# Optimization experiments

Measured on AMD Instinct MI355X. Metric: run time of the kernel, lower is better.

Reference implementation:

```python
import jax, jax.numpy as jnp
import numpy as np

B, N, C = 2, 2048, 768
H = 12
D = C // H
SCALE = D ** -0.5
EPS = 1e-5
HID = 4 * C


def layer_norm(x, g, b):
    mu = jnp.mean(x, axis=-1, keepdims=True)
    var = jnp.var(x, axis=-1, keepdims=True)
    return (x - mu) * jax.lax.rsqrt(var + EPS) * g + b


def setup_inputs():
    key = jax.random.key(0)
    ks = jax.random.split(key, 12)
    s = C ** -0.5
    x = jax.random.normal(ks[0], (B, N, C), dtype=jnp.float32)
    mask = (jax.random.uniform(ks[1], (B, N, N)) < 0.1).astype(jnp.float32)
    return {
        "x": x,
        "mask": mask,
        "g1": jnp.ones((C,), jnp.float32),
        "b1": jnp.zeros((C,), jnp.float32),
        "Wq": jax.random.normal(ks[2], (C, C), jnp.float32) * s,
        "Wkv": jax.random.normal(ks[3], (2 * C, C), jnp.float32) * s,
        "Wp": jax.random.normal(ks[4], (C, C), jnp.float32) * s,
        "bp": jnp.zeros((C,), jnp.float32),
        "g2": jnp.ones((C,), jnp.float32),
        "b2": jnp.zeros((C,), jnp.float32),
        "W1": jax.random.normal(ks[5], (HID, C), jnp.float32) * s,
        "bf1": jnp.zeros((HID,), jnp.float32),
        "W2": jax.random.normal(ks[6], (C, HID), jnp.float32) * (HID ** -0.5),
        "bf2": jnpmp if False else jnp.zeros((C,), jnp.float32),
    }


def block_fwd(x, mask, g1, b1, Wq, Wkv, Wp, bp, g2, b2, W1, bf1, W2, bf2):
    # --- attention branch (pre-norm) ---
    xn = layer_norm(x, g1, b1)
    q = (xn @ Wq.T).reshape(B, N, H, D).transpose(0, 2, 1, 3)      # bhnd
    kv = (xn @ Wkv.T).reshape(B, N, 2, H, D).transpose(2, 0, 3, 1, 4)
    k, v = kv[0], kv[1]                                             # bhnd
    attn = jnp.einsum('bhnd,bhmd->bhnm', q, k) * SCALE
    attn = attn + (mask * -100000.0)[:, None]                       # additive mask
    attn = jax.nn.softmax(attn, axis=-1)
    o = jnp.einsum('bhnm,bhmd->bhnd', attn, v)
    o = o.transpose(0, 2, 1, 3).reshape(B, N, C)
    o = o @ Wp.T + bp
    x = x + o
    # --- MLP branch (pre-norm) ---
    xn2 = layer_norm(x, g2, b2)
    h = jax.nn.gelu(xn2 @ W1.T + bf1, approximate=False)
    x = x + (h @ W2.T + bf2)
    return x


def reference(x, mask, g1, b1, Wq, Wkv, Wp, bp, g2, b2, W1, bf1, W2, bf2):
    return block_fwd(x, mask, g1, b1, Wq, Wkv, Wp, bp, g2, b2, W1, bf1, W2, bf2)
```

## Files before the change

### kernel.cpp

```cpp
#include <hip/hip_runtime.h>
#include <hip/hip_bf16.h>
#include <cstdint>
#include <cstddef>

#define BB 2
#define NN 2048
#define CC 768
#define HH 12
#define DD 64
#define HID 3072
#define TT (BB*NN)

typedef __attribute__((ext_vector_type(8))) short bf16x8;
typedef __attribute__((ext_vector_type(4))) short bf16x4;
typedef __attribute__((ext_vector_type(4))) float f32x4;

__device__ __forceinline__ unsigned short f2bf(float f) {
    unsigned int u = __float_as_uint(f);
    u += 0x7fffu + ((u >> 16) & 1u);
    return (unsigned short)(u >> 16);
}
__device__ __forceinline__ float bf2f(unsigned short u) {
    return __uint_as_float(((unsigned int)u) << 16);
}
#if __has_builtin(__builtin_amdgcn_exp2f)
#define EXP2F(x) __builtin_amdgcn_exp2f(x)
#else
#define EXP2F(x) exp2f(x)
#endif

__device__ __forceinline__ void gload16(const void* g, void* l) {
    __builtin_amdgcn_global_load_lds((__attribute__((address_space(1))) unsigned int*)g,
                                     (__attribute__((address_space(3))) unsigned int*)l,
                                     16, 0, 0);
}

#define WAITV(N) asm volatile("s_waitcnt vmcnt(" #N ")" ::: "memory")
#define WAITLGKM asm volatile("s_waitcnt lgkmcnt(0)" ::: "memory")

struct CvtArgs {
    const float* in[5];
    unsigned short* out[5];
    int n4[5];
};
typedef __attribute__((ext_vector_type(4))) float float4v;
typedef __attribute__((ext_vector_type(4))) unsigned short ushort4v;
__global__ __launch_bounds__(256) void cvt5_kernel(CvtArgs a) {
    int base = blockIdx.x * 256 + threadIdx.x;
    int stride = gridDim.x * 256;
#pragma unroll
    for (int s = 0; s < 5; ++s) {
        const float4v* ip = (const float4v*)a.in[s];
        ushort4v* op = (ushort4v*)a.out[s];
        for (int i = base; i < a.n4[s]; i += stride) {
            float4v v = ip[i];
            ushort4v o;
            o[0] = f2bf(v[0]); o[1] = f2bf(v[1]); o[2] = f2bf(v[2]); o[3] = f2bf(v[3]);
            op[i] = o;
        }
    }
}

__global__ __launch_bounds__(256) void maskbits_kernel(const float* __restrict__ mask,
                                                       unsigned short* __restrict__ mb, int n) {
    int i = blockIdx.x * 256 + threadIdx.x;
    if (i >= n) return;
    const float4v* mp = (const float4v*)(mask + (size_t)i * 16);
    unsigned int bits = 0;
#pragma unroll
    for (int q = 0; q < 4; ++q) {
        float4v v = mp[q];
#pragma unroll
        for (int j = 0; j < 4; ++j) bits |= (v[j] > 0.5f) ? (1u << (q * 4 + j)) : 0u;
    }
    mb[i] = (unsigned short)bits;
}

__global__ __launch_bounds__(256) void ln_kernel(const float* __restrict__ x,
                                                 const float* __restrict__ g,
                                                 const float* __restrict__ b,
                                                 unsigned short* __restrict__ out) {
    int t = blockIdx.x;
    int tid = threadIdx.x;
    const float* xr = x + (size_t)t * CC;
    float v0 = xr[tid], v1 = xr[tid + 256], v2 = xr[tid + 512];
    float s = v0 + v1 + v2;
    float s2 = v0 * v0 + v1 * v1 + v2 * v2;
#pragma unroll
    for (int off = 1; off < 64; off <<= 1) {
        s  += __shfl_xor(s, off);
        s2 += __shfl_xor(s2, off);
    }
    __shared__ float red[8];
    int wv = tid >> 6, lane = tid & 63;
    if (lane == 0) { red[wv] = s; red[wv + 4] = s2; }
    __syncthreads();
    s  = red[0] + red[1] + red[2] + red[3];
    s2 = red[4] + red[5] + red[6] + red[7];
    float mu   = s * (1.0f / CC);
    float var  = s2 * (1.0f / CC) - mu * mu;
    float rstd = rsqrtf(var + 1e-5f);
    unsigned short* orow = out + (size_t)t * CC;
    orow[tid]       = f2bf((v0 - mu) * rstd * g[tid]       + b[tid]);
    orow[tid + 256] = f2bf((v1 - mu) * rstd * g[tid + 256] + b[tid + 256]);
    orow[tid + 512] = f2bf((v2 - mu) * rstd * g[tid + 512] + b[tid + 512]);
}

template <int EPI, int BM>
__global__ __launch_bounds__(256) void gemm_bt(const unsigned short* __restrict__ A,
                                               const unsigned short* __restrict__ Bw,
                                               const float* __restrict__ bias,
                                               const float* __restrict__ res,
                                               void* __restrict__ out,
                                               int M, int N, int K) {
    constexpr int MI = BM / 32;
    constexpr int NCA = (BM * 4) / 256;
    __shared__ alignas(16) unsigned short As[2][BM * 32];
    __shared__ alignas(16) unsigned short Bs[2][128 * 32];
    int tid = threadIdx.x;
    int lane = tid & 63, wv = tid >> 6;
    int l16 = lane & 15, lg = lane >> 4;
    int bm = blockIdx.x, bn = blockIdx.y;
    int wm = (wv & 1) * (BM / 2), wn = (wv >> 1) * 64;

    const unsigned short* Ab = A + (size_t)bm * BM * K;
    const unsigned short* Bb = Bw + (size_t)bn * 128 * K;

    const unsigned short* aSrc[NCA]; int aDst[NCA];
#pragma unroll
    for (int i = 0; i < NCA; ++i) {
        int c = tid + i * 256;
        int row = c >> 2, p = c & 3;
        int lc = p ^ ((row >> 1) & 3);
        aSrc[i] = Ab + (size_t)row * K + lc * 8;
        aDst[i] = c * 8;
    }
    const unsigned short* bSrc[2]; int bDst[2];
#pragma unroll
    for (int i = 0; i < 2; ++i) {
        int c = tid + i * 256;
        int row = c >> 2, p = c & 3;
        int lc = p ^ ((row >> 1) & 3);
        bSrc[i] = Bb + (size_t)row * K + lc * 8;
        bDst[i] = c * 8;
    }
    int aoff = (wm + l16) * 32 + ((lg ^ (((wm + l16) >> 1) & 3)) * 8);
    int boff = (wn + l16) * 32 + ((lg ^ (((wn + l16) >> 1) & 3)) * 8);

    f32x4 acc[MI][4];
#pragma unroll
    for (int i = 0; i < MI; ++i)
#pragma unroll
        for (int j = 0; j < 4; ++j) acc[i][j] = f32x4{0.f, 0.f, 0.f, 0.f};

    auto STAGE = [&](int s, int k0) {
#pragma unroll
        for (int i = 0; i < NCA; ++i) gload16(aSrc[i] + k0, &As[s][aDst[i]]);
#pragma unroll
        for (int i = 0; i < 2; ++i)   gload16(bSrc[i] + k0, &Bs[s][bDst[i]]);
    };

    STAGE(0, 0);
    int nt = K / 32;
    for (int t = 0; t < nt; ++t) {
        int cur = t & 1;
        if (t + 1 < nt) {
            STAGE(cur ^ 1, (t + 1) * 32);
            if constexpr (NCA + 2 == 4) { WAITV(4); } else { WAITV(3); }
        } else {
            WAITV(0);
        }
        __builtin_amdgcn_s_barrier();
        bf16x8 af[MI], bfr[4];
#pragma unroll
        for (int mi = 0; mi < MI; ++mi) af[mi]  = *(const bf16x8*)&As[cur][aoff + mi * 512];
#pragma unroll
        for (int ni = 0; ni < 4; ++ni)  bfr[ni] = *(const bf16x8*)&Bs[cur][boff + ni * 512];
#pragma unroll
        for (int mi = 0; mi < MI; ++mi)
#pragma unroll
            for (int ni = 0; ni < 4; ++ni)
                acc[mi][ni] = __builtin_amdgcn_mfma_f32_16x16x32_bf16(bfr[ni], af[mi], acc[mi][ni], 0, 0, 0);
        WAITLGKM;
        __builtin_amdgcn_s_barrier();
    }

#pragma unroll
    for (int mi = 0; mi < MI; ++mi) {
        int row = bm * BM + wm + mi * 16 + l16;
#pragma unroll
        for (int ni = 0; ni < 4; ++ni) {
            int col = bn * 128 + wn + ni * 16 + lg * 4;
            size_t idx = (size_t)row * N + col;
            f32x4 v = acc[mi][ni];
            if (EPI == 0) {
                bf16x4 ov;
#pragma unroll
                for (int r = 0; r < 4; ++r) ov[r] = (short)f2bf(v[r]);
                *(bf16x4*)((unsigned short*)out + idx) = ov;
            } else if (EPI == 1 || EPI == 3) {
                f32x4 bv = *(const f32x4*)&bias[col];
                f32x4 rv = *(const f32x4*)&res[idx];
                f32x4 ov;
#pragma unroll
                for (int r = 0; r < 4; ++r) ov[r] = v[r] + bv[r] + rv[r];
                *(f32x4*)((float*)out + idx) = ov;
            } else {
                f32x4 bv = *(const f32x4*)&bias[col];
                bf16x4 ov;
#pragma unroll
                for (int r = 0; r < 4; ++r) {
                    float t2 = v[r] + bv[r];
                    t2 = 0.5f * t2 * (1.0f + erff(t2 * 0.70710678118f));
                    ov[r] = (short)f2bf(t2);
                }
                *(bf16x4*)((unsigned short*)out + idx) = ov;
            }
        }
    }
}

#define KVB 64
#define ANT (NN/KVB)
#define VP 68
__global__ __launch_bounds__(256, 4) void attn_kernel(const unsigned short* __restrict__ qkv,
                                                      const unsigned short* __restrict__ maskb,
                                                      unsigned short* __restrict__ o) {
    __shared__ alignas(16) unsigned short Ks[2][64 * 64];
    __shared__ alignas(16) unsigned short Vt[2][64 * VP];
    int tid = threadIdx.x;
    int lane = tid & 63, wv = tid >> 6;
    int l16 = lane & 15, lg = lane >> 4;
    int qb = blockIdx.x;
    int bh = blockIdx.y;
    int b = bh / HH, h = bh % HH;
    int qrow = qb * 64 + wv * 16 + l16;

    const unsigned short* qp = qkv + ((size_t)(b * NN + qrow)) * 2304 + h * DD;
    bf16x8 q0r = *(const bf16x8*)(qp + 8 * lg);
    bf16x8 q1r = *(const bf16x8*)(qp + 32 + 8 * lg);
    const float QSC = 0.125f * 1.4426950408889634f;
    bf16x8 q0, q1;
#pragma unroll
    for (int j = 0; j < 8; ++j) {
        q0[j] = (short)f2bf(bf2f((unsigned short)q0r[j]) * QSC);
        q1[j] = (short)f2bf(bf2f((unsigned short)q1r[j]) * QSC);
    }

    const unsigned short* mrow  = maskb + ((size_t)(b * NN + qrow)) * 128;
    const unsigned short* kbase = qkv + (size_t)b * NN * 2304 + 768 + h * DD;
    const unsigned short* vbase = qkv + (size_t)b * NN * 2304 + 1536 + h * DD;

    const unsigned short* kSrc[2]; int kDst[2];
#pragma unroll
    for (int i = 0; i < 2; ++i) {
        int c = tid + i * 256;
        int row = c >> 3, p = c & 7;
        int lc = p ^ (row & 7);
        kSrc[i] = kbase + (size_t)row * 2304 + lc * 8;
        kDst[i] = c * 8;
    }
    int kp = tid & 31, dg = tid >> 5;
    const unsigned short* vSrc = vbase + (size_t)(2 * kp) * 2304 + dg * 8;

    int sw = l16 & 7;
    int kb0 = l16 * 64 + ((lg ^ sw) * 8);
    int kb1 = l16 * 64 + (((lg + 4) ^ sw) * 8);
    int vbo = l16 * VP + lg * 4;

    bf16x8 va, vb;
    unsigned long long mb_cur, mb_nxt;

    f32x4 oa[4];
#pragma unroll
    for (int i = 0; i < 4; ++i) oa[i] = f32x4{0.f, 0.f, 0.f, 0.f};
    float mrun = -INFINITY, lrun = 0.f;

    auto LOAD = [&](int t, int s) {
#pragma unroll
        for (int i = 0; i < 2; ++i) gload16(kSrc[i] + (size_t)t * KVB * 2304, &Ks[s][kDst[i]]);
        const unsigned short* vp = vSrc + (size_t)t * KVB * 2304;
        va = *(const bf16x8*)(vp);
        vb = *(const bf16x8*)(vp + 2304);
        mb_nxt = *(const unsigned long long*)(mrow + t * 4);
    };
    auto WRITEV = [&](int s) {
        unsigned int* VtU = (unsigned int*)Vt[s];
#pragma unroll
        for (int j = 0; j < 8; ++j)
            VtU[(dg * 8 + j) * (VP / 2) + kp] =
                (unsigned int)(unsigned short)va[j] | ((unsigned int)(unsigned short)vb[j] << 16);
    };

    LOAD(0, 0);
    WRITEV(0);
    mb_cur = mb_nxt;
    __syncthreads();
    int cur = 0;

    for (int kt = 0; kt < ANT; ++kt) {
        bool pre = (kt + 1 < ANT);
        if (pre) LOAD(kt + 1, cur ^ 1);
        const unsigned short* Ksc = Ks[cur];
        const unsigned short* Vtc = Vt[cur];

        float sv[16];
#pragma unroll
        for (int ks = 0; ks < 4; ++ks) {
            bf16x8 k0 = *(const bf16x8*)&Ksc[kb0 + ks * 1024];
            bf16x8 k1 = *(const bf16x8*)&Ksc[kb1 + ks * 1024];
            f32x4 sa = f32x4{0.f, 0.f, 0.f, 0.f};
            sa = __builtin_amdgcn_mfma_f32_16x16x32_bf16(k0, q0, sa, 0, 0, 0);
            sa = __builtin_amdgcn_mfma_f32_16x16x32_bf16(k1, q1, sa, 0, 0, 0);
            unsigned int m16 = (unsigned int)(mb_cur >> (ks * 16 + lg * 4));
#pragma unroll
            for (int r = 0; r < 4; ++r) {
                float mbit = (float)((m16 >> r) & 1u);
                sv[ks * 4 + r] = fmaf(mbit, -144269.5f, sa[r]);
            }
        }
        float tmax = sv[0];
#pragma unroll
        for (int i = 1; i < 16; ++i) tmax = fmaxf(tmax, sv[i]);
        tmax = fmaxf(tmax, __shfl_xor(tmax, 16));
        tmax = fmaxf(tmax, __shfl_xor(tmax, 32));

        if (__any(tmax > mrun + 11.5f)) {
            float mnew = fmaxf(mrun, tmax);
            float sc = EXP2F(mrun - mnew);
            lrun *= sc;
#pragma unroll
            for (int db = 0; db < 4; ++db) {
                oa[db][0] *= sc; oa[db][1] *= sc; oa[db][2] *= sc; oa[db][3] *= sc;
            }
            mrun = mnew;
        }

        float ps = 0.f;
        bf16x4 pf[4];
#pragma unroll
        for (int ks = 0; ks < 4; ++ks)
#pragma unroll
            for (int r = 0; r < 4; ++r) {
                float p = EXP2F(sv[ks * 4 + r] - mrun);
                ps += p;
                pf[ks][r] = (short)f2bf(p);
            }
        lrun += ps;

#pragma unroll
        for (int ks = 0; ks < 4; ++ks)
#pragma unroll
            for (int db = 0; db < 4; ++db) {
                bf16x4 vf = *(const bf16x4*)&Vtc[vbo + db * 16 * VP + ks * 16];
                oa[db] = __builtin_amdgcn_mfma_f32_16x16x16bf16_1k(vf, pf[ks], oa[db], 0, 0, 0);
            }

        if (pre) WRITEV(cur ^ 1);
        __syncthreads();
        if (pre) { cur ^= 1; mb_cur = mb_nxt; }
    }

    float lt = lrun;
    lt += __shfl_xor(lt, 16);
    lt += __shfl_xor(lt, 32);
    float inv = 1.0f / lt;
    unsigned short* op = o + ((size_t)(b * NN + qrow)) * CC + h * DD;
#pragma unroll
    for (int db = 0; db < 4; ++db) {
        bf16x4 ov;
#pragma unroll
        for (int r = 0; r < 4; ++r) ov[r] = (short)f2bf(oa[db][r] * inv);
        *(bf16x4*)&op[db * 16 + lg * 4] = ov;
    }
}

extern "C" void kernel_launch(void* const* d_in, const int* in_sizes, int n_in,
                              void* d_out, int out_size, void* d_ws, size_t ws_size,
                              hipStream_t stream) {
    const float* x    = (const float*)d_in[0];
    const float* mask = (const float*)d_in[1];
    const float* g1   = (const float*)d_in[2];
    const float* b1   = (const float*)d_in[3];
    const float* Wq   = (const float*)d_in[4];
    const float* Wkv  = (const float*)d_in[5];
    const float* Wp   = (const float*)d_in[6];
    const float* bp   = (const float*)d_in[7];
    const float* g2   = (const float*)d_in[8];
    const float* b2   = (const float*)d_in[9];
    const float* W1   = (const float*)d_in[10];
    const float* bf1  = (const float*)d_in[11];
    const float* W2   = (const float*)d_in[12];
    const float* bf2  = (const float*)d_in[13];
    float* out = (float*)d_out;

    char* w = (char*)d_ws;
    unsigned short* wqkv = (unsigned short*)w;      w += (size_t)2304 * 768 * 2;
    unsigned short* wp   = (unsigned short*)w;      w += (size_t)768 * 768 * 2;
    unsigned short* w1   = (unsigned short*)w;      w += (size_t)3072 * 768 * 2;
    unsigned short* w2   = (unsigned short*)w;      w += (size_t)768 * 3072 * 2;
    unsigned short* xn   = (unsigned short*)w;      w += (size_t)TT * CC * 2;
    unsigned short* qkv  = (unsigned short*)w;      w += (size_t)TT * 2304 * 2;
    unsigned short* mb   = (unsigned short*)w;      w += (size_t)BB * NN * 128 * 2;
    unsigned short* obuf = (unsigned short*)w;      w += (size_t)TT * CC * 2;
    float*          x1   = (float*)w;               w += (size_t)TT * CC * 4;
    unsigned short* xn2  = (unsigned short*)w;      w += (size_t)TT * CC * 2;
    unsigned short* hbuf = (unsigned short*)w;      w += (size_t)TT * HID * 2;

    CvtArgs ca;
    ca.in[0] = Wq;  ca.out[0] = wqkv;             ca.n4[0] = 768 * 768 / 4;
    ca.in[1] = Wkv; ca.out[1] = wqkv + 768 * 768; ca.n4[1] = 1536 * 768 / 4;
    ca.in[2] = Wp;  ca.out[2] = wp;               ca.n4[2] = 768 * 768 / 4;
    ca.in[3] = W1;  ca.out[3] = w1;               ca.n4[3] = 3072 * 768 / 4;
    ca.in[4] = W2;  ca.out[4] = w2;               ca.n4[4] = 768 * 3072 / 4;
    cvt5_kernel<<<1024, 256, 0, stream>>>(ca);

    {
        int n = BB * NN * (NN / 16);
        maskbits_kernel<<<(n + 255) / 256, 256, 0, stream>>>(mask, mb, n);
    }

    ln_kernel<<<TT, 256, 0, stream>>>(x, g1, b1, xn);

    gemm_bt<0, 128><<<dim3(TT / 128, 2304 / 128), 256, 0, stream>>>(xn, wqkv, nullptr, nullptr, qkv, TT, 2304, 768);

    attn_kernel<<<dim3(NN / 64, BB * HH), 256, 0, stream>>>(qkv, mb, obuf);

    gemm_bt<1, 64><<<dim3(TT / 64, 768 / 128), 256, 0, stream>>>(obuf, wp, bp, x, x1, TT, 768, 768);

    ln_kernel<<<TT, 256, 0, stream>>>(x1, g2, b2, xn2);

    gemm_bt<2, 128><<<dim3(TT / 128, HID / 128), 256, 0, stream>>>(xn2, w1, bf1, nullptr, hbuf, TT, HID, 768);

    gemm_bt<3, 64><<<dim3(TT / 64, 768 / 128), 256, 0, stream>>>(hbuf, w2, bf2, x1, out, TT, 768, HID);
}
```

Before: 219.9 us.

## Double GEMM K-tile to 64 with 8-way swizzle and XCD-aware block remapping

The GEMM K tile grows from 32 to 64, with LDS buffers and the XOR swizzle widened to 8 chunks. This halves the number of barrier/wait iterations per K loop. Both GEMM and attention grids become 1D with a remap that keeps neighbouring row tiles (or heads) on the same XCD, improving L2 reuse of shared operand tiles. The larger LDS footprint may reduce occupancy.

```diff
diff --git a/kernel.cpp b/kernel.cpp
--- a/kernel.cpp
+++ b/kernel.cpp
@@ -113,14 +113,21 @@
                                                const float* __restrict__ res,
                                                void* __restrict__ out,
                                                int M, int N, int K) {
-    constexpr int MI = BM / 32;
-    constexpr int NCA = (BM * 4) / 256;
-    __shared__ alignas(16) unsigned short As[2][BM * 32];
-    __shared__ alignas(16) unsigned short Bs[2][128 * 32];
+    constexpr int MI  = BM / 32;
+    constexpr int NCA = BM / 32;
+    constexpr int NCB = 4;
+    __shared__ alignas(16) unsigned short As[2][BM * 64];
+    __shared__ alignas(16) unsigned short Bs[2][128 * 64];
     int tid = threadIdx.x;
     int lane = tid & 63, wv = tid >> 6;
     int l16 = lane & 15, lg = lane >> 4;
-    int bm = blockIdx.x, bn = blockIdx.y;
+
+    int BMT = M / BM, chunk = BMT >> 3;
+    int id = blockIdx.x;
+    int xcd = id & 7, r = id >> 3;
+    int bm = xcd * chunk + (r % chunk);
+    int bn = r / chunk;
+
     int wm = (wv & 1) * (BM / 2), wn = (wv >> 1) * 64;
 
     const unsigned short* Ab = A + (size_t)bm * BM * K;
@@ -130,22 +137,27 @@
 #pragma unroll
     for (int i = 0; i < NCA; ++i) {
         int c = tid + i * 256;
-        int row = c >> 2, p = c & 3;
-        int lc = p ^ ((row >> 1) & 3);
+        int row = c >> 3, p = c & 7;
+        int lc = p ^ (row & 7);
         aSrc[i] = Ab + (size_t)row * K + lc * 8;
         aDst[i] = c * 8;
     }
-    const unsigned short* bSrc[2]; int bDst[2];
-#pragma unroll
-    for (int i = 0; i < 2; ++i) {
+    const unsigned short* bSrc[NCB]; int bDst[NCB];
+#pragma unroll
+    for (int i = 0; i < NCB; ++i) {
         int c = tid + i * 256;
-        int row = c >> 2, p = c & 3;
-        int lc = p ^ ((row >> 1) & 3);
+        int row = c >> 3, p = c & 7;
+        int lc = p ^ (row & 7);
         bSrc[i] = Bb + (size_t)row * K + lc * 8;
         bDst[i] = c * 8;
     }
-    int aoff = (wm + l16) * 32 + ((lg ^ (((wm + l16) >> 1) & 3)) * 8);
-    int boff = (wn + l16) * 32 + ((lg ^ (((wn + l16) >> 1) & 3)) * 8);
+    int arow = wm + l16, brow = wn + l16;
+    int aoff[2], boff[2];
+#pragma unroll
+    for (int ks = 0; ks < 2; ++ks) {
+        aoff[ks] = arow * 64 + (((ks * 4 + lg) ^ (arow & 7)) * 8);
+        boff[ks] = brow * 64 + (((ks * 4 + lg) ^ (brow & 7)) * 8);
+    }
 
     f32x4 acc[MI][4];
 #pragma unroll
@@ -157,30 +169,33 @@
 #pragma unroll
         for (int i = 0; i < NCA; ++i) gload16(aSrc[i] + k0, &As[s][aDst[i]]);
 #pragma unroll
-        for (int i = 0; i < 2; ++i)   gload16(bSrc[i] + k0, &Bs[s][bDst[i]]);
+        for (int i = 0; i < NCB; ++i) gload16(bSrc[i] + k0, &Bs[s][bDst[i]]);
     };
 
     STAGE(0, 0);
-    int nt = K / 32;
+    int nt = K / 64;
     for (int t = 0; t < nt; ++t) {
         int cur = t & 1;
         if (t + 1 < nt) {
-            STAGE(cur ^ 1, (t + 1) * 32);
-            if constexpr (NCA + 2 == 4) { WAITV(4); } else { WAITV(3); }
+            STAGE(cur ^ 1, (t + 1) * 64);
+            if constexpr (BM == 128) { WAITV(8); } else { WAITV(6); }
         } else {
             WAITV(0);
         }
         __builtin_amdgcn_s_barrier();
-        bf16x8 af[MI], bfr[4];
-#pragma unroll
-        for (int mi = 0; mi < MI; ++mi) af[mi]  = *(const bf16x8*)&As[cur][aoff + mi * 512];
-#pragma unroll
-        for (int ni = 0; ni < 4; ++ni)  bfr[ni] = *(const bf16x8*)&Bs[cur][boff + ni * 512];
-#pragma unroll
-        for (int mi = 0; mi < MI; ++mi)
-#pragma unroll
-            for (int ni = 0; ni < 4; ++ni)
-                acc[mi][ni] = __builtin_amdgcn_mfma_f32_16x16x32_bf16(bfr[ni], af[mi], acc[mi][ni], 0, 0, 0);
+#pragma unroll
+        for (int ks = 0; ks < 2; ++ks) {
+            bf16x8 af[MI], bfr[4];
+#pragma unroll
+            for (int mi = 0; mi < MI; ++mi) af[mi]  = *(const bf16x8*)&As[cur][aoff[ks] + mi * 1024];
+#pragma unroll
+            for (int ni = 0; ni < 4; ++ni)  bfr[ni] = *(const bf16x8*)&Bs[cur][boff[ks] + ni * 1024];
+#pragma unroll
+            for (int mi = 0; mi < MI; ++mi)
+#pragma unroll
+                for (int ni = 0; ni < 4; ++ni)
+                    acc[mi][ni] = __builtin_amdgcn_mfma_f32_16x16x32_bf16(bfr[ni], af[mi], acc[mi][ni], 0, 0, 0);
+        }
         WAITLGKM;
         __builtin_amdgcn_s_barrier();
     }
@@ -196,23 +211,23 @@
             if (EPI == 0) {
                 bf16x4 ov;
 #pragma unroll
-                for (int r = 0; r < 4; ++r) ov[r] = (short)f2bf(v[r]);
+                for (int r2 = 0; r2 < 4; ++r2) ov[r2] = (short)f2bf(v[r2]);
                 *(bf16x4*)((unsigned short*)out + idx) = ov;
             } else if (EPI == 1 || EPI == 3) {
                 f32x4 bv = *(const f32x4*)&bias[col];
                 f32x4 rv = *(const f32x4*)&res[idx];
                 f32x4 ov;
 #pragma unroll
-                for (int r = 0; r < 4; ++r) ov[r] = v[r] + bv[r] + rv[r];
+                for (int r2 = 0; r2 < 4; ++r2) ov[r2] = v[r2] + bv[r2] + rv[r2];
                 *(f32x4*)((float*)out + idx) = ov;
             } else {
                 f32x4 bv = *(const f32x4*)&bias[col];
                 bf16x4 ov;
 #pragma unroll
-                for (int r = 0; r < 4; ++r) {
-                    float t2 = v[r] + bv[r];
+                for (int r2 = 0; r2 < 4; ++r2) {
+                    float t2 = v[r2] + bv[r2];
                     t2 = 0.5f * t2 * (1.0f + erff(t2 * 0.70710678118f));
-                    ov[r] = (short)f2bf(t2);
+                    ov[r2] = (short)f2bf(t2);
                 }
                 *(bf16x4*)((unsigned short*)out + idx) = ov;
             }
@@ -231,8 +246,10 @@
     int tid = threadIdx.x;
     int lane = tid & 63, wv = tid >> 6;
     int l16 = lane & 15, lg = lane >> 4;
-    int qb = blockIdx.x;
-    int bh = blockIdx.y;
+    int id = blockIdx.x;
+    int xcd = id & 7, r = id >> 3;
+    int bh = xcd * 3 + (r % 3);
+    int qb = r / 3;
     int b = bh / HH, h = bh % HH;
     int qrow = qb * 64 + wv * 16 + l16;
 
@@ -314,9 +331,9 @@
             sa = __builtin_amdgcn_mfma_f32_16x16x32_bf16(k1, q1, sa, 0, 0, 0);
             unsigned int m16 = (unsigned int)(mb_cur >> (ks * 16 + lg * 4));
 #pragma unroll
-            for (int r = 0; r < 4; ++r) {
-                float mbit = (float)((m16 >> r) & 1u);
-                sv[ks * 4 + r] = fmaf(mbit, -144269.5f, sa[r]);
+            for (int r2 = 0; r2 < 4; ++r2) {
+                float mbit = (float)((m16 >> r2) & 1u);
+                sv[ks * 4 + r2] = fmaf(mbit, -144269.5f, sa[r2]);
             }
         }
         float tmax = sv[0];
@@ -341,10 +358,10 @@
 #pragma unroll
         for (int ks = 0; ks < 4; ++ks)
 #pragma unroll
-            for (int r = 0; r < 4; ++r) {
-                float p = EXP2F(sv[ks * 4 + r] - mrun);
+            for (int r2 = 0; r2 < 4; ++r2) {
+                float p = EXP2F(sv[ks * 4 + r2] - mrun);
                 ps += p;
-                pf[ks][r] = (short)f2bf(p);
+                pf[ks][r2] = (short)f2bf(p);
             }
         lrun += ps;
 
@@ -370,7 +387,7 @@
     for (int db = 0; db < 4; ++db) {
         bf16x4 ov;
 #pragma unroll
-        for (int r = 0; r < 4; ++r) ov[r] = (short)f2bf(oa[db][r] * inv);
+        for (int r2 = 0; r2 < 4; ++r2) ov[r2] = (short)f2bf(oa[db][r2] * inv);
         *(bf16x4*)&op[db * 16 + lg * 4] = ov;
     }
 }
@@ -422,15 +439,15 @@
 
     ln_kernel<<<TT, 256, 0, stream>>>(x, g1, b1, xn);
 
-    gemm_bt<0, 128><<<dim3(TT / 128, 2304 / 128), 256, 0, stream>>>(xn, wqkv, nullptr, nullptr, qkv, TT, 2304, 768);
-
-    attn_kernel<<<dim3(NN / 64, BB * HH), 256, 0, stream>>>(qkv, mb, obuf);
-
-    gemm_bt<1, 64><<<dim3(TT / 64, 768 / 128), 256, 0, stream>>>(obuf, wp, bp, x, x1, TT, 768, 768);
+    gemm_bt<0, 128><<<32 * 18, 256, 0, stream>>>(xn, wqkv, nullptr, nullptr, qkv, TT, 2304, 768);
+
+    attn_kernel<<<32 * 24, 256, 0, stream>>>(qkv, mb, obuf);
+
+    gemm_bt<1, 64><<<64 * 6, 256, 0, stream>>>(obuf, wp, bp, x, x1, TT, 768, 768);
 
     ln_kernel<<<TT, 256, 0, stream>>>(x1, g2, b2, xn2);
 
-    gemm_bt<2, 128><<<dim3(TT / 128, HID / 128), 256, 0, stream>>>(xn2, w1, bf1, nullptr, hbuf, TT, HID, 768);
-
-    gemm_bt<3, 64><<<dim3(TT / 64, 768 / 128), 256, 0, stream>>>(hbuf, w2, bf2, x1, out, TT, 768, HID);
-}
+    gemm_bt<2, 128><<<32 * 24, 256, 0, stream>>>(xn2, w1, bf1, nullptr, hbuf, TT, HID, 768);
+
+    gemm_bt<3, 64><<<64 * 6, 256, 0, stream>>>(hbuf, w2, bf2, x1, out, TT, 768, HID);
+}
```

Result: no change. 223.1 us (+1.5%).
